# Kernel optimization log

Hardware: AMD Instinct MI355X
Metric: run time of the kernel (lower is better)

Reference implementation:

```python
import jax, jax.numpy as jnp
import numpy as np

MAX_DISP = 4  # max_displacement
PAD = MAX_DISP
ODIM = 2 * MAX_DISP + 1  # 9 -> 81 cost-volume channels


def setup_inputs() -> dict:
    key = jax.random.key(0)
    k1, k2 = jax.random.split(key)
    B, C, H, W = 4, 256, 96, 192
    x1 = jax.random.normal(k1, (B, C, H, W), dtype=jnp.float32)
    x2 = jax.random.normal(k2, (B, C, H, W), dtype=jnp.float32)
    return {"x1": x1, "x2": x2}


def reference(x1, x2):
    B, C, H, W = x1.shape
    # zero-pad x2 spatially by PAD on each side (matches F.pad([pad]*4))
    x2p = jnp.pad(x2, ((0, 0), (0, 0), (PAD, PAD), (PAD, PAD)))
    cv = []
    for i in range(ODIM):          # fixed 9x9 displacement grid
        for j in range(ODIM):
            shifted = jax.lax.dynamic_slice(
                x2p, (0, 0, i, j), (B, C, H, W))
            # mean over channel dim -> [B, H, W]
            cv.append(jnp.mean(x1 * shifted, axis=1))
    return jnp.stack(cv, axis=1)  # [B, 81, H, W]
```

## Files before the change

### kernel.cpp

```cpp
#include <hip/hip_runtime.h>
#include <stddef.h>


#define NB 4
#define NC 256
#define HH 96
#define WW 192
#define TW 16
#define TH 8
#define KC 32
#define NROWS 16

#define KS 264
#define RS 1096
#define XBI(row, kg, n) ((row) * RS + (kg) * KS + (n) * 8)

typedef __attribute__((ext_vector_type(8))) short bf16x8;
typedef __attribute__((ext_vector_type(4))) float f32x4;

__device__ __forceinline__ unsigned short f2bf(float f) {
    union { float f; unsigned u; } c; c.f = f;
    unsigned r = c.u + 0x7FFFu + ((c.u >> 16) & 1u);
    return (unsigned short)(r >> 16);
}

__global__ __launch_bounds__(512, 1) void corr_mfma(
    const float* __restrict__ x1, const float* __restrict__ x2,
    float* __restrict__ out)
{
    __shared__ union {
        unsigned short xb[NROWS * RS];
        float band[TH][9][9][18];
    } lds;

    const int tid  = threadIdx.x;
    const int wv   = tid >> 6;
    const int lane = tid & 63;
    const int col  = lane & 15;
    const int q    = lane >> 4;
    const int w0   = blockIdx.x * TW;
    const int h0   = blockIdx.y * TH;
    const int b    = blockIdx.z;
    const int h    = h0 + wv;

    f32x4 acc[9][2];
#pragma unroll
    for (int di = 0; di < 9; ++di) {
        acc[di][0] = (f32x4)0.0f;
        acc[di][1] = (f32x4)0.0f;
    }

    float pf[24];
    float pa[8];

#define STAGE_LOAD(kc_)                                                        \
    {                                                                          \
        const int kcv = (kc_);                                                 \
        _Pragma("unroll")                                                      \
        for (int k = 0; k < 3; ++k) {                                          \
            int t   = tid + k * 512;                                           \
            int seg = t % 6;                                                   \
            int row = (t / 6) & 15;                                            \
            int cp  = t / 96;                                                  \
            int gh  = h0 - 4 + row;                                            \
            int gw  = w0 - 4 + seg * 4;                                        \
            bool ok = (gh >= 0) & (gh < HH) & (gw >= 0) & (gw <= WW - 4);      \
            _Pragma("unroll")                                                  \
            for (int e = 0; e < 2; ++e) {                                      \
                float4 ld = make_float4(0.f, 0.f, 0.f, 0.f);                   \
                if (ok) {                                                      \
                    size_t idx = ((size_t)((b * NC + kcv + cp * 2 + e) * HH + gh)) * WW + gw; \
                    ld = *(const float4*)&x2[idx];                             \
                }                                                              \
                *(float4*)&pf[(k * 2 + e) * 4] = ld;                           \
            }                                                                  \
        }                                                                      \
    }

#define X1_LOAD(kc_)                                                           \
    {                                                                          \
        const int kcv = (kc_);                                                 \
        _Pragma("unroll")                                                      \
        for (int j = 0; j < 8; ++j) {                                          \
            size_t idx = ((size_t)((b * NC + kcv + q * 8 + j) * HH + h)) * WW + w0 + col; \
            pa[j] = x1[idx];                                                   \
        }                                                                      \
    }

    STAGE_LOAD(0);
    X1_LOAD(0);

    for (int ci = 0; ci < 8; ++ci) {
#pragma unroll
        for (int k = 0; k < 3; ++k) {
            int t   = tid + k * 512;
            int seg = t % 6;
            int row = (t / 6) & 15;
            int cp  = t / 96;
            int kg  = cp >> 2;
            int k0  = (cp & 3) * 2;
#pragma unroll
            for (int p = 0; p < 4; ++p) {
                ushort2 v;
                v.x = f2bf(pf[(k * 2 + 0) * 4 + p]);
                v.y = f2bf(pf[(k * 2 + 1) * 4 + p]);
                *(ushort2*)&lds.xb[XBI(row, kg, seg * 4 + p) + k0] = v;
            }
        }
        __syncthreads();

        bf16x8 a;
#pragma unroll
        for (int j = 0; j < 8; ++j) a[j] = (short)f2bf(pa[j]);

        if (ci < 7) {
            STAGE_LOAD((ci + 1) * KC);
            X1_LOAD((ci + 1) * KC);
        }

#pragma unroll
        for (int di = 0; di < 9; ++di) {
            int r = wv + di;
            bf16x8 b0 = *(const bf16x8*)&lds.xb[XBI(r, q, col)];
            bf16x8 b1 = *(const bf16x8*)&lds.xb[XBI(r, q, col + 16)];
            acc[di][0] = __builtin_amdgcn_mfma_f32_16x16x32_bf16(a, b0, acc[di][0], 0, 0, 0);
            acc[di][1] = __builtin_amdgcn_mfma_f32_16x16x32_bf16(a, b1, acc[di][1], 0, 0, 0);
        }
        __syncthreads();
    }

#pragma unroll
    for (int di = 0; di < 9; ++di)
#pragma unroll
        for (int half = 0; half < 2; ++half)
#pragma unroll
            for (int r = 0; r < 4; ++r) {
                int m  = q * 4 + r;
                int dj = half * 16 + col - m;
                if (dj >= 0 && dj < 9)
                    lds.band[wv][di][dj][m] = acc[di][half][r];
            }
    __syncthreads();

    const float scale = 1.0f / 256.0f;
#pragma unroll
    for (int it = 0; it < 21; ++it) {
        int combo = it * 4 + q;
        if (combo < 81) {
            float v = lds.band[wv][combo / 9][combo % 9][col];
            out[((size_t)((b * 81 + combo) * HH + h)) * WW + w0 + col] = v * scale;
        }
    }
}

extern "C" void kernel_launch(void* const* d_in, const int* in_sizes, int n_in,
                              void* d_out, int out_size, void* d_ws, size_t ws_size,
                              hipStream_t stream) {
    const float* x1 = (const float*)d_in[0];
    const float* x2 = (const float*)d_in[1];
    float* out = (float*)d_out;

    dim3 grid(WW / TW, HH / TH, NB);
    corr_mfma<<<grid, 512, 0, stream>>>(x1, x2, out);
}
```

Baseline: 243.8 us.

## Swizzle block order, precompute load offsets, raise occupancy, remap staging threads

Changes launch bounds to allow up to 4 blocks per CU. Flattens the grid to 1D and swizzles block indices so neighbouring tiles land on different XCD groups. Precomputes global and LDS offsets once and advances them by a fixed stride, removing per-iteration index arithmetic. Remaps staging threads so channel pairs vary fastest within a row, and issues the next x2 prefetch before the barrier. Capping registers for higher occupancy risks spilling the 72 accumulator registers, and LDS usage (~35KB) may itself limit concurrency.

```diff
diff --git a/kernel.cpp b/kernel.cpp
--- a/kernel.cpp
+++ b/kernel.cpp
@@ -10,6 +10,8 @@
 #define TH 8
 #define KC 32
 #define NROWS 16
+#define CHW (HH * WW)
+#define KSTRIDE (KC * CHW)
 
 #define KS 264
 #define RS 1096
@@ -24,7 +26,7 @@
     return (unsigned short)(r >> 16);
 }
 
-__global__ __launch_bounds__(512, 1) void corr_mfma(
+__global__ __launch_bounds__(512, 4) void corr_mfma(
     const float* __restrict__ x1, const float* __restrict__ x2,
     float* __restrict__ out)
 {
@@ -33,14 +35,20 @@
         float band[TH][9][9][18];
     } lds;
 
+    const int lin = blockIdx.x;
+    const int sw  = (lin & 7) * 72 + (lin >> 3);
+    const int b   = sw / 144;
+    const int t2  = sw - b * 144;
+    const int ty  = t2 / 12;
+    const int tx  = t2 - ty * 12;
+
     const int tid  = threadIdx.x;
     const int wv   = tid >> 6;
     const int lane = tid & 63;
     const int col  = lane & 15;
     const int q    = lane >> 4;
-    const int w0   = blockIdx.x * TW;
-    const int h0   = blockIdx.y * TH;
-    const int b    = blockIdx.z;
+    const int w0   = tx * TW;
+    const int h0   = ty * TH;
     const int h    = h0 + wv;
 
     f32x4 acc[9][2];
@@ -50,79 +58,78 @@
         acc[di][1] = (f32x4)0.0f;
     }
 
+    unsigned o2k[3];
+    int      lofk[3];
+    bool     okk[3];
+#pragma unroll
+    for (int k = 0; k < 3; ++k) {
+        const int t   = tid + k * 512;
+        const int seg = t % 6;
+        const int u   = t / 6;
+        const int cp  = u & 15;
+        const int row = u >> 4;
+        const int gh  = h0 - 4 + row;
+        const int gw  = w0 - 4 + seg * 4;
+        okk[k] = (gh >= 0) & (gh < HH) & (gw >= 0) & (gw <= WW - 4);
+        const int ghc = gh < 0 ? 0 : (gh > HH - 1 ? HH - 1 : gh);
+        const int gwc = gw < 0 ? 0 : gw;
+        o2k[k]  = (unsigned)(((b * NC + cp * 2) * HH + ghc) * WW + gwc);
+        lofk[k] = XBI(row, cp >> 2, seg * 4) + (cp & 3) * 2;
+    }
+    unsigned o1 = (unsigned)(((b * NC + q * 8) * HH + h) * WW + w0 + col);
+
     float pf[24];
     float pa[8];
 
-#define STAGE_LOAD(kc_)                                                        \
-    {                                                                          \
-        const int kcv = (kc_);                                                 \
-        _Pragma("unroll")                                                      \
-        for (int k = 0; k < 3; ++k) {                                          \
-            int t   = tid + k * 512;                                           \
-            int seg = t % 6;                                                   \
-            int row = (t / 6) & 15;                                            \
-            int cp  = t / 96;                                                  \
-            int gh  = h0 - 4 + row;                                            \
-            int gw  = w0 - 4 + seg * 4;                                        \
-            bool ok = (gh >= 0) & (gh < HH) & (gw >= 0) & (gw <= WW - 4);      \
-            _Pragma("unroll")                                                  \
-            for (int e = 0; e < 2; ++e) {                                      \
-                float4 ld = make_float4(0.f, 0.f, 0.f, 0.f);                   \
-                if (ok) {                                                      \
-                    size_t idx = ((size_t)((b * NC + kcv + cp * 2 + e) * HH + gh)) * WW + gw; \
-                    ld = *(const float4*)&x2[idx];                             \
-                }                                                              \
-                *(float4*)&pf[(k * 2 + e) * 4] = ld;                           \
-            }                                                                  \
-        }                                                                      \
+#define STAGE_LOAD()                                                     \
+    {                                                                    \
+        _Pragma("unroll")                                                \
+        for (int k = 0; k < 3; ++k) {                                    \
+            _Pragma("unroll")                                            \
+            for (int e = 0; e < 2; ++e) {                                \
+                float4 ld = make_float4(0.f, 0.f, 0.f, 0.f);             \
+                if (okk[k]) ld = *(const float4*)&x2[o2k[k] + e * CHW];  \
+                *(float4*)&pf[(k * 2 + e) * 4] = ld;                     \
+            }                                                            \
+            o2k[k] += KSTRIDE;                                           \
+        }                                                                \
     }
 
-#define X1_LOAD(kc_)                                                           \
-    {                                                                          \
-        const int kcv = (kc_);                                                 \
-        _Pragma("unroll")                                                      \
-        for (int j = 0; j < 8; ++j) {                                          \
-            size_t idx = ((size_t)((b * NC + kcv + q * 8 + j) * HH + h)) * WW + w0 + col; \
-            pa[j] = x1[idx];                                                   \
-        }                                                                      \
+#define X1_LOAD()                                                        \
+    {                                                                    \
+        _Pragma("unroll")                                                \
+        for (int j = 0; j < 8; ++j) pa[j] = x1[o1 + j * CHW];            \
+        o1 += KSTRIDE;                                                   \
     }
 
-    STAGE_LOAD(0);
-    X1_LOAD(0);
+    STAGE_LOAD();
+    X1_LOAD();
+
+    const int rbase = XBI(wv, q, col);
 
     for (int ci = 0; ci < 8; ++ci) {
 #pragma unroll
         for (int k = 0; k < 3; ++k) {
-            int t   = tid + k * 512;
-            int seg = t % 6;
-            int row = (t / 6) & 15;
-            int cp  = t / 96;
-            int kg  = cp >> 2;
-            int k0  = (cp & 3) * 2;
 #pragma unroll
             for (int p = 0; p < 4; ++p) {
                 ushort2 v;
                 v.x = f2bf(pf[(k * 2 + 0) * 4 + p]);
                 v.y = f2bf(pf[(k * 2 + 1) * 4 + p]);
-                *(ushort2*)&lds.xb[XBI(row, kg, seg * 4 + p) + k0] = v;
+                *(ushort2*)&lds.xb[lofk[k] + p * 8] = v;
             }
         }
+        if (ci < 7) STAGE_LOAD();
         __syncthreads();
 
         bf16x8 a;
 #pragma unroll
         for (int j = 0; j < 8; ++j) a[j] = (short)f2bf(pa[j]);
-
-        if (ci < 7) {
-            STAGE_LOAD((ci + 1) * KC);
-            X1_LOAD((ci + 1) * KC);
-        }
+        if (ci < 7) X1_LOAD();
 
 #pragma unroll
         for (int di = 0; di < 9; ++di) {
-            int r = wv + di;
-            bf16x8 b0 = *(const bf16x8*)&lds.xb[XBI(r, q, col)];
-            bf16x8 b1 = *(const bf16x8*)&lds.xb[XBI(r, q, col + 16)];
+            bf16x8 b0 = *(const bf16x8*)&lds.xb[rbase + di * RS];
+            bf16x8 b1 = *(const bf16x8*)&lds.xb[rbase + di * RS + 128];
             acc[di][0] = __builtin_amdgcn_mfma_f32_16x16x32_bf16(a, b0, acc[di][0], 0, 0, 0);
             acc[di][1] = __builtin_amdgcn_mfma_f32_16x16x32_bf16(a, b1, acc[di][1], 0, 0, 0);
         }
@@ -160,6 +167,6 @@
     const float* x2 = (const float*)d_in[1];
     float* out = (float*)d_out;
 
-    dim3 grid(WW / TW, HH / TH, NB);
+    dim3 grid(576);
     corr_mfma<<<grid, 512, 0, stream>>>(x1, x2, out);
 }
```

After: 220.9 us. 9.4% less time.
